# Performance work log

Measured on AMD Instinct MI355X. Metric: run time of the kernel, lower is better.

## Reference

```python
import jax, jax.numpy as jnp
from jax import lax
import numpy as np

QMIN, QMAX = -127.0, 127.0
STRIDE = (1, 1)
PADDING = ((1, 1), (1, 1))
DILATION = (1, 1)
DN = ('NCHW', 'OIHW', 'NCHW')


def _quantize_x(x, scale_x):
    # symmetric static per-tensor int8 quantization
    return jnp.clip(jnp.round(x / scale_x), QMIN, QMAX)


def _quantize_w(w):
    # symmetric dynamic per-output-channel int8 quantization
    scale_w = jnp.max(jnp.abs(w), axis=(1, 2, 3), keepdims=True) / QMAX  # [O,1,1,1]
    q_w = jnp.clip(jnp.round(w / scale_w), QMIN, QMAX)
    return q_w, scale_w


def setup_inputs() -> dict:
    key = jax.random.key(0)
    kx, kw, kb = jax.random.split(key, 3)
    B, C, H, W = 32, 128, 56, 56
    O, kH, kW = 256, 3, 3
    x = jax.random.normal(kx, (B, C, H, W), jnp.float32)
    weight = jax.random.normal(kw, (O, C, kH, kW), jnp.float32) * 0.05
    bias = jax.random.normal(kb, (O,), jnp.float32)
    scale_x = jnp.asarray(0.02, jnp.float32)  # static per-tensor scale buffer
    # exact int8 product lookup table: lut[a+127, b+127] = a*b
    v = np.arange(-127, 128, dtype=np.int32)
    lut = jnp.asarray(v[:, None] * v[None, :])
    return {"x": x, "weight": weight, "bias": bias, "scale_x": scale_x, "lut": lut}


def reference(x, weight, bias, scale_x, lut):
    # lut holds the exact int8 product table, so bgemm_int8(q_x, q_w, lut) is an
    # exact integer GEMM; im2col + bGEMM == conv of quantized tensors.
    q_x = _quantize_x(x, scale_x)            # [B,C,H,W] integer-valued fp32
    q_w, scale_w = _quantize_w(weight)       # [O,C,kH,kW], [O,1,1,1]
    acc = lax.conv_general_dilated(
        q_x, q_w, STRIDE, PADDING, rhs_dilation=DILATION, dimension_numbers=DN
    )                                        # [B,O,OH,OW] integer-valued accumulator
    out = acc * scale_x * scale_w.reshape(1, -1, 1, 1)  # per-channel dequant
    return out + bias.reshape(1, -1, 1, 1)
```

## Files before the change

kernel.cpp:

```cpp
#include <hip/hip_runtime.h>


#define BATCH 32
#define CIN   128
#define HH    56
#define WW    56
#define OCH   256

typedef __attribute__((ext_vector_type(4))) int int4v;
typedef __attribute__((ext_vector_type(2))) long longx2;

#define QX_BYTES (32 * 56 * 56 * 128)
#define QW_BYTES (256 * 1152)
#define WS_NEEDED (QX_BYTES + QW_BYTES + 1024)

__device__ __forceinline__ void gload_lds16(const void* g, void* l) {
  __builtin_amdgcn_global_load_lds(
      (const __attribute__((address_space(1))) unsigned int*)g,
      (__attribute__((address_space(3))) unsigned int*)l, 16, 0, 0);
}

__global__ __launch_bounds__(256) void quant_w_kernel(
    const float* __restrict__ w, const float* __restrict__ sxp,
    char* __restrict__ qwf, float* __restrict__ alpha) {
  __shared__ float wf[1152];
  __shared__ float red[256];
  const int o = blockIdx.x;
  const int tid = threadIdx.x;
  const float* wrow = w + (size_t)o * 1152;
  float m = 0.f;
  for (int i = tid; i < 288; i += 256) {
    const float4 v = ((const float4*)wrow)[i];
    ((float4*)wf)[i] = v;
    m = fmaxf(m, fmaxf(fmaxf(fabsf(v.x), fabsf(v.y)),
                       fmaxf(fabsf(v.z), fabsf(v.w))));
  }
  red[tid] = m;
  __syncthreads();
  for (int s = 128; s > 0; s >>= 1) {
    if (tid < s) red[tid] = fmaxf(red[tid], red[tid + s]);
    __syncthreads();
  }
  const float sc = red[0] / 127.0f;
  if (tid == 0) alpha[o] = sc * sxp[0];
  if (tid < 36) {
    const int r = tid >> 2, c04 = tid & 3;
    const int og = o >> 5, t = (o >> 4) & 1, l16 = o & 15;
    unsigned int* base = (unsigned int*)(qwf + (size_t)og * 36864 +
                                         (size_t)(r * 4 + c04) * 1024);
#pragma unroll
    for (int quad = 0; quad < 4; ++quad) {
#pragma unroll
      for (int half = 0; half < 2; ++half) {
        unsigned int pk = 0;
#pragma unroll
        for (int k = 0; k < 4; ++k) {
          const int c = c04 * 32 + quad * 8 + half * 4 + k;
          const int q =
              (int)fminf(127.f, fmaxf(-127.f, rintf(wf[c * 9 + r] / sc)));
          pk |= ((unsigned int)(q & 255)) << (8 * k);
        }
        base[(l16 * 4 + quad) * 4 + t * 2 + half] = pk;
      }
    }
  }
}

__global__ __launch_bounds__(256) void quant_x_kernel(
    const float* __restrict__ x, const float* __restrict__ sxp,
    unsigned int* __restrict__ qxp) {
  __shared__ char ldsA[128 * 60];
  const int row = blockIdx.x;
  const int b = row / 56, h = row % 56;
  const float sx = sxp[0];
  for (int i = threadIdx.x; i < 1792; i += 256) {
    const int c = i / 14, f = i % 14;
    const float4 v =
        *(const float4*)(x + (((size_t)b * 128 + c) * 56 + h) * 56 + 4 * f);
    unsigned int pk;
    pk  = (unsigned int)((int)fminf(127.f, fmaxf(-127.f, rintf(v.x / sx))) & 255);
    pk |= ((unsigned int)((int)fminf(127.f, fmaxf(-127.f, rintf(v.y / sx))) & 255)) << 8;
    pk |= ((unsigned int)((int)fminf(127.f, fmaxf(-127.f, rintf(v.z / sx))) & 255)) << 16;
    pk |= ((unsigned int)((int)fminf(127.f, fmaxf(-127.f, rintf(v.w / sx))) & 255)) << 24;
    *(unsigned int*)(ldsA + c * 60 + 4 * f) = pk;
  }
  __syncthreads();
  unsigned int* orow = qxp + (size_t)row * 56 * 32;
  for (int i = threadIdx.x; i < 1792; i += 256) {
    const int w = i >> 5, jd = i & 31;
    const int c0 = (jd ^ (((w + 1) & 15) << 1)) << 2;
    unsigned int pk = 0;
#pragma unroll
    for (int k = 0; k < 4; ++k)
      pk |= ((unsigned int)(unsigned char)ldsA[(c0 + k) * 60 + w]) << (8 * k);
    orow[i] = pk;
  }
}

#define XSLAB 8448

__global__ __launch_bounds__(256, 6) void conv_kernel(
    const char* __restrict__ qxp, const char* __restrict__ qwf,
    const float* __restrict__ alpha, const float* __restrict__ bias,
    float* __restrict__ out) {
  __shared__ __attribute__((aligned(16))) char Xs8[3 * XSLAB];

  const int id = blockIdx.x;
  const int xcd = id & 7;
  int kk = id >> 3;
  const int yy = (kk >= 224) ? 1 : 0;
  kk -= yy * 224;
  const int bi = xcd * 224 + kk;
  const int b  = bi / 56;
  const int oh = bi % 56;
  const int o0 = yy * 128;
  const int tid = threadIdx.x;
  const int wave = tid >> 6, lane = tid & 63;
  const int l16 = lane & 15, quad = lane >> 4;

  int m_r[4], n_r[4];
  {
    int4v zz = {0, 0, 0, 0};
    long a1 = 0, b1 = 0, a2 = 0, b2 = 0;
    if (quad == 0) {
      a1 = 1L;
      b1 = (long)(l16 + 1);
      a2 = (long)(l16 + 1);
      b2 = 1L;
    }
    int4v d1 = __builtin_amdgcn_mfma_i32_16x16x32_i8(a1, b1, zz, 0, 0, 0);
    int4v d2 = __builtin_amdgcn_mfma_i32_16x16x32_i8(a2, b2, zz, 0, 0, 0);
#pragma unroll
    for (int r = 0; r < 4; ++r) {
      n_r[r] = (d1[r] - 1) & 15;
      m_r[r] = (d2[r] - 1) & 15;
    }
  }

  const longx2* wb2 = (const longx2*)(qwf + (size_t)(yy * 4 + wave) * 36864) +
                      (l16 * 4 + quad);
  longx2 ap[2][4];
#pragma unroll
  for (int c04 = 0; c04 < 4; ++c04) ap[0][c04] = wb2[(size_t)c04 * 64];

  for (int kh = 0; kh < 3; ++kh) {
    const int ih = oh - 1 + kh;
    char* slab = Xs8 + kh * XSLAB;
    if (ih >= 0 && ih < HH) {
      const char* src = qxp + ((size_t)b * 56 + ih) * 7168;
      for (int i = tid; i < 448; i += 256)
        gload_lds16(src + i * 16, slab + 128 + i * 16);
      for (int i = tid; i < 320; i += 256) {
        const int cg = i >> 5, dw = i & 31;
        const int col = (cg == 0) ? 0 : 56 + cg;
        ((unsigned int*)slab)[col * 32 + dw] = 0u;
      }
    } else {
      for (int i = tid; i < 2112; i += 256) ((unsigned int*)slab)[i] = 0u;
    }
  }

  int4v acc[2][4];
#pragma unroll
  for (int t = 0; t < 2; ++t)
#pragma unroll
    for (int u = 0; u < 4; ++u) acc[t][u] = (int4v){0, 0, 0, 0};

  __syncthreads();

#pragma unroll
  for (int g = 0; g < 9; ++g) {
    const int kh = g / 3, kw = g % 3;
    if (g < 8) {
#pragma unroll
      for (int c04 = 0; c04 < 4; ++c04)
        ap[(g + 1) & 1][c04] = wb2[(size_t)((g + 1) * 4 + c04) * 64];
    }
    const char* Xk = Xs8 + kh * XSLAB;
    const int ph = ((l16 + kw) & 15) << 3;
#pragma unroll
    for (int c04 = 0; c04 < 4; ++c04) {
      const int boff = (c04 * 32 + quad * 8) ^ ph;
      long bop[4];
#pragma unroll
      for (int u = 0; u < 4; ++u)
        bop[u] = *(const long*)(Xk + (u * 16 + l16 + kw) * 128 + boff);
#pragma unroll
      for (int u = 0; u < 4; ++u) {
        acc[0][u] = __builtin_amdgcn_mfma_i32_16x16x32_i8(
            ap[g & 1][c04][0], bop[u], acc[0][u], 0, 0, 0);
        acc[1][u] = __builtin_amdgcn_mfma_i32_16x16x32_i8(
            ap[g & 1][c04][1], bop[u], acc[1][u], 0, 0, 0);
      }
    }
  }

#pragma unroll
  for (int t = 0; t < 2; ++t) {
#pragma unroll
    for (int u = 0; u < 4; ++u) {
#pragma unroll
      for (int r = 0; r < 4; ++r) {
        const int ol = wave * 32 + t * 16 + m_r[r];
        const int ow = u * 16 + n_r[r];
        if (ow < WW) {
          const int oo = o0 + ol;
          out[(((size_t)b * OCH + oo) * HH + oh) * WW + ow] =
              (float)acc[t][u][r] * alpha[oo] + bias[oo];
        }
      }
    }
  }
}

#define FAS_ROW 392
#define FXS_ROW 136
#define FLDS_XS (128 * FAS_ROW)
#define FLDS_SC (FLDS_XS + 66 * FXS_ROW)
#define FLDS_AL (FLDS_SC + 512)
#define FLDS_BI (FLDS_AL + 512)
#define FLDS_RED (FLDS_BI + 512)
#define FLDS_TOT (FLDS_RED + 1024)

__global__ __launch_bounds__(256) void conv_fused_kernel(
    const float* __restrict__ x, const float* __restrict__ w,
    const float* __restrict__ bias, const float* __restrict__ sxp,
    float* __restrict__ out) {
  __shared__ __attribute__((aligned(16))) char lds[FLDS_TOT];
  char* As8 = lds;
  char* Xs8 = lds + FLDS_XS;
  float* scaleS = (float*)(lds + FLDS_SC);
  float* alphaS = (float*)(lds + FLDS_AL);
  float* biasS  = (float*)(lds + FLDS_BI);
  float* red    = (float*)(lds + FLDS_RED);

  const int bi = blockIdx.x;
  const int b  = bi / 56;
  const int oh = bi % 56;
  const int o0 = blockIdx.y * 128;
  const int tid = threadIdx.x;
  const int wave = tid >> 6, lane = tid & 63;
  const int l16 = lane & 15, quad = lane >> 4;
  const float sx = sxp[0];

  int m_r[4], n_r[4];
  {
    int4v zz = {0, 0, 0, 0};
    long a1 = 0, b1 = 0, a2 = 0, b2 = 0;
    if (quad == 0) { a1 = 1L; b1 = (long)(l16 + 1); a2 = (long)(l16 + 1); b2 = 1L; }
    int4v d1 = __builtin_amdgcn_mfma_i32_16x16x32_i8(a1, b1, zz, 0, 0, 0);
    int4v d2 = __builtin_amdgcn_mfma_i32_16x16x32_i8(a2, b2, zz, 0, 0, 0);
#pragma unroll
    for (int r = 0; r < 4; ++r) { n_r[r] = (d1[r] - 1) & 15; m_r[r] = (d2[r] - 1) & 15; }
  }
  {
    const int o = tid >> 1, half = tid & 1;
    const float4* p = (const float4*)(w + (size_t)(o0 + o) * 1152 + half * 576);
    float m = 0.f;
#pragma unroll 4
    for (int i = 0; i < 144; ++i) {
      const float4 v = p[i];
      m = fmaxf(m, fmaxf(fmaxf(fabsf(v.x), fabsf(v.y)), fmaxf(fabsf(v.z), fabsf(v.w))));
    }
    red[tid] = m;
  }
  __syncthreads();
  {
    const int o = tid >> 1;
    if ((tid & 1) == 0) {
      const float sc = fmaxf(red[2 * o], red[2 * o + 1]) / 127.0f;
      scaleS[o] = sc; alphaS[o] = sc * sx; biasS[o] = bias[o0 + o];
    }
  }
  int4v acc[2][4];
#pragma unroll
  for (int t = 0; t < 2; ++t)
#pragma unroll
    for (int u = 0; u < 4; ++u) acc[t][u] = (int4v){0, 0, 0, 0};

  for (int kh = 0; kh < 3; ++kh) {
    const int ih = oh - 1 + kh;
    const bool row_ok = (ih >= 0) && (ih < HH);
    __syncthreads();
    for (int idx = tid; idx < 66 * 128; idx += 256) {
      const int col = idx % 66, c = idx / 66, iw = col - 1;
      int q = 0;
      if (row_ok && iw >= 0 && iw < WW) {
        const float xv = x[(((size_t)b * CIN + c) * HH + ih) * WW + iw];
        q = (int)fminf(127.f, fmaxf(-127.f, rintf(xv / sx)));
      }
      Xs8[col * FXS_ROW + c] = (char)q;
    }
    for (int idx = tid; idx < 16384; idx += 256) {
      const int c = idx & 127, o = idx >> 7;
      const float s = scaleS[o];
      const float* wp = w + (size_t)(o0 + o) * 1152 + c * 9 + kh * 3;
#pragma unroll
      for (int kw = 0; kw < 3; ++kw) {
        const int q = (int)fminf(127.f, fmaxf(-127.f, rintf(wp[kw] / s)));
        As8[o * FAS_ROW + kw * 128 + c] = (char)q;
      }
    }
    __syncthreads();
    const int obase = wave * 32;
#pragma unroll
    for (int kw = 0; kw < 3; ++kw) {
#pragma unroll
      for (int c0 = 0; c0 < 128; c0 += 32) {
        long aop[2], bop[4];
#pragma unroll
        for (int t = 0; t < 2; ++t)
          aop[t] = *(const long*)(As8 + (obase + t * 16 + l16) * FAS_ROW + kw * 128 + c0 + quad * 8);
#pragma unroll
        for (int u = 0; u < 4; ++u)
          bop[u] = *(const long*)(Xs8 + (u * 16 + l16 + kw) * FXS_ROW + c0 + quad * 8);
#pragma unroll
        for (int t = 0; t < 2; ++t)
#pragma unroll
          for (int u = 0; u < 4; ++u)
            acc[t][u] = __builtin_amdgcn_mfma_i32_16x16x32_i8(aop[t], bop[u], acc[t][u], 0, 0, 0);
      }
    }
  }
#pragma unroll
  for (int t = 0; t < 2; ++t) {
#pragma unroll
    for (int u = 0; u < 4; ++u) {
#pragma unroll
      for (int r = 0; r < 4; ++r) {
        const int ol = wave * 32 + t * 16 + m_r[r];
        const int ow = u * 16 + n_r[r];
        if (ow < WW)
          out[(((size_t)b * OCH + o0 + ol) * HH + oh) * WW + ow] =
              (float)acc[t][u][r] * alphaS[ol] + biasS[ol];
      }
    }
  }
}

extern "C" void kernel_launch(void* const* d_in, const int* in_sizes, int n_in,
                              void* d_out, int out_size, void* d_ws, size_t ws_size,
                              hipStream_t stream) {
  const float *x = nullptr, *w = nullptr, *bias = nullptr, *sx = nullptr;
  for (int i = 0; i < n_in; ++i) {
    const int s = in_sizes[i];
    if (s == BATCH * CIN * HH * WW) x = (const float*)d_in[i];
    else if (s == OCH * CIN * 9)    w = (const float*)d_in[i];
    else if (s == OCH)              bias = (const float*)d_in[i];
    else if (s == 1)                sx = (const float*)d_in[i];
  }
  if (!x || !w || !bias || !sx) {
    x = (const float*)d_in[0]; w = (const float*)d_in[1];
    bias = (const float*)d_in[2]; sx = (const float*)d_in[3];
  }
  float* out = (float*)d_out;

  if (ws_size >= (size_t)WS_NEEDED) {
    unsigned int* qxp = (unsigned int*)d_ws;
    char* qwf = (char*)d_ws + QX_BYTES;
    float* alpha = (float*)((char*)d_ws + QX_BYTES + QW_BYTES);
    quant_w_kernel<<<OCH, 256, 0, stream>>>(w, sx, qwf, alpha);
    quant_x_kernel<<<BATCH * HH, 256, 0, stream>>>(x, sx, qxp);
    conv_kernel<<<BATCH * HH * 2, 256, 0, stream>>>(
        (const char*)qxp, qwf, alpha, bias, out);
  } else {
    conv_fused_kernel<<<dim3(BATCH * HH, 2), 256, 0, stream>>>(x, w, bias, sx, out);
  }
}
```

Measured before the change: 196.9 us.

## Switch conv to 32x32x32 int8 MFMA with full-channel blocks and new weight layout

Replaces the 16x16x32 int8 MFMA tiles with 32x32x32 int8 MFMA. Each block now computes all 256 output channels for one output row, so the grid is halved and each input slab is loaded into LDS once instead of twice. The packed weight layout in quant_w_kernel changes to match the new A-operand fragment, and launch bounds drop to 3 blocks per CU. Each wave now holds 64 channels and 64 accumulator registers, which raises register pressure and reduces the number of resident blocks.

```diff
diff --git a/kernel.cpp b/kernel.cpp
--- a/kernel.cpp
+++ b/kernel.cpp
@@ -8,6 +8,7 @@
 #define OCH   256
 
 typedef __attribute__((ext_vector_type(4))) int int4v;
+typedef __attribute__((ext_vector_type(16))) int int16v;
 typedef __attribute__((ext_vector_type(2))) long longx2;
 
 #define QX_BYTES (32 * 56 * 56 * 128)
@@ -43,26 +44,24 @@
   }
   const float sc = red[0] / 127.0f;
   if (tid == 0) alpha[o] = sc * sxp[0];
-  if (tid < 36) {
-    const int r = tid >> 2, c04 = tid & 3;
-    const int og = o >> 5, t = (o >> 4) & 1, l16 = o & 15;
-    unsigned int* base = (unsigned int*)(qwf + (size_t)og * 36864 +
-                                         (size_t)(r * 4 + c04) * 1024);
-#pragma unroll
-    for (int quad = 0; quad < 4; ++quad) {
-#pragma unroll
-      for (int half = 0; half < 2; ++half) {
-        unsigned int pk = 0;
-#pragma unroll
-        for (int k = 0; k < 4; ++k) {
-          const int c = c04 * 32 + quad * 8 + half * 4 + k;
-          const int q =
-              (int)fminf(127.f, fmaxf(-127.f, rintf(wf[c * 9 + r] / sc)));
-          pk |= ((unsigned int)(q & 255)) << (8 * k);
-        }
-        base[(l16 * 4 + quad) * 4 + t * 2 + half] = pk;
-      }
-    }
+  if (tid < 72) {
+    const int r = tid >> 3, cs = (tid >> 1) & 3, hi = tid & 1;
+    const int ot = o >> 5, ml = o & 31;
+    int4v pk;
+#pragma unroll
+    for (int d = 0; d < 4; ++d) {
+      unsigned int p = 0;
+#pragma unroll
+      for (int k = 0; k < 4; ++k) {
+        const int c = cs * 32 + hi * 16 + d * 4 + k;
+        const int q =
+            (int)fminf(127.f, fmaxf(-127.f, rintf(wf[c * 9 + r] / sc)));
+        p |= ((unsigned int)(q & 255)) << (8 * k);
+      }
+      pk[d] = (int)p;
+    }
+    *(int4v*)(qwf +
+              ((((size_t)ot * 9 + r) * 4 + cs) * 64 + ml + 32 * hi) * 16) = pk;
   }
 }
 
@@ -99,7 +98,7 @@
 
 #define XSLAB 8448
 
-__global__ __launch_bounds__(256, 6) void conv_kernel(
+__global__ __launch_bounds__(256, 3) void conv_kernel(
     const char* __restrict__ qxp, const char* __restrict__ qwf,
     const float* __restrict__ alpha, const float* __restrict__ bias,
     float* __restrict__ out) {
@@ -107,41 +106,12 @@
 
   const int id = blockIdx.x;
   const int xcd = id & 7;
-  int kk = id >> 3;
-  const int yy = (kk >= 224) ? 1 : 0;
-  kk -= yy * 224;
-  const int bi = xcd * 224 + kk;
+  const int bi = xcd * 224 + (id >> 3);
   const int b  = bi / 56;
   const int oh = bi % 56;
-  const int o0 = yy * 128;
   const int tid = threadIdx.x;
   const int wave = tid >> 6, lane = tid & 63;
-  const int l16 = lane & 15, quad = lane >> 4;
-
-  int m_r[4], n_r[4];
-  {
-    int4v zz = {0, 0, 0, 0};
-    long a1 = 0, b1 = 0, a2 = 0, b2 = 0;
-    if (quad == 0) {
-      a1 = 1L;
-      b1 = (long)(l16 + 1);
-      a2 = (long)(l16 + 1);
-      b2 = 1L;
-    }
-    int4v d1 = __builtin_amdgcn_mfma_i32_16x16x32_i8(a1, b1, zz, 0, 0, 0);
-    int4v d2 = __builtin_amdgcn_mfma_i32_16x16x32_i8(a2, b2, zz, 0, 0, 0);
-#pragma unroll
-    for (int r = 0; r < 4; ++r) {
-      n_r[r] = (d1[r] - 1) & 15;
-      m_r[r] = (d2[r] - 1) & 15;
-    }
-  }
-
-  const longx2* wb2 = (const longx2*)(qwf + (size_t)(yy * 4 + wave) * 36864) +
-                      (l16 * 4 + quad);
-  longx2 ap[2][4];
-#pragma unroll
-  for (int c04 = 0; c04 < 4; ++c04) ap[0][c04] = wb2[(size_t)c04 * 64];
+  const int l31 = lane & 31, hi = lane >> 5;
 
   for (int kh = 0; kh < 3; ++kh) {
     const int ih = oh - 1 + kh;
@@ -160,11 +130,22 @@
     }
   }
 
-  int4v acc[2][4];
-#pragma unroll
-  for (int t = 0; t < 2; ++t)
-#pragma unroll
-    for (int u = 0; u < 4; ++u) acc[t][u] = (int4v){0, 0, 0, 0};
+  const int4v* wb = (const int4v*)qwf;
+  const int ot0 = wave * 2;
+  int4v ap[2][2][4];
+#pragma unroll
+  for (int ot = 0; ot < 2; ++ot)
+#pragma unroll
+    for (int cs = 0; cs < 4; ++cs)
+      ap[0][ot][cs] = wb[(((size_t)(ot0 + ot) * 9 + 0) * 4 + cs) * 64 + lane];
+
+  int16v acc[2][2];
+#pragma unroll
+  for (int ot = 0; ot < 2; ++ot)
+#pragma unroll
+    for (int u = 0; u < 2; ++u)
+#pragma unroll
+      for (int r = 0; r < 16; ++r) acc[ot][u][r] = 0;
 
   __syncthreads();
 
@@ -173,41 +154,48 @@
     const int kh = g / 3, kw = g % 3;
     if (g < 8) {
 #pragma unroll
-      for (int c04 = 0; c04 < 4; ++c04)
-        ap[(g + 1) & 1][c04] = wb2[(size_t)((g + 1) * 4 + c04) * 64];
+      for (int ot = 0; ot < 2; ++ot)
+#pragma unroll
+        for (int cs = 0; cs < 4; ++cs)
+          ap[(g + 1) & 1][ot][cs] =
+              wb[(((size_t)(ot0 + ot) * 9 + (g + 1)) * 4 + cs) * 64 + lane];
     }
     const char* Xk = Xs8 + kh * XSLAB;
-    const int ph = ((l16 + kw) & 15) << 3;
-#pragma unroll
-    for (int c04 = 0; c04 < 4; ++c04) {
-      const int boff = (c04 * 32 + quad * 8) ^ ph;
-      long bop[4];
-#pragma unroll
-      for (int u = 0; u < 4; ++u)
-        bop[u] = *(const long*)(Xk + (u * 16 + l16 + kw) * 128 + boff);
-#pragma unroll
-      for (int u = 0; u < 4; ++u) {
-        acc[0][u] = __builtin_amdgcn_mfma_i32_16x16x32_i8(
-            ap[g & 1][c04][0], bop[u], acc[0][u], 0, 0, 0);
-        acc[1][u] = __builtin_amdgcn_mfma_i32_16x16x32_i8(
-            ap[g & 1][c04][1], bop[u], acc[1][u], 0, 0, 0);
-      }
-    }
-  }
-
-#pragma unroll
-  for (int t = 0; t < 2; ++t) {
-#pragma unroll
-    for (int u = 0; u < 4; ++u) {
-#pragma unroll
-      for (int r = 0; r < 4; ++r) {
-        const int ol = wave * 32 + t * 16 + m_r[r];
-        const int ow = u * 16 + n_r[r];
-        if (ow < WW) {
-          const int oo = o0 + ol;
-          out[(((size_t)b * OCH + oo) * HH + oh) * WW + ow] =
-              (float)acc[t][u][r] * alpha[oo] + bias[oo];
-        }
+    const int ph = ((l31 + kw) & 15) << 3;
+#pragma unroll
+    for (int cs = 0; cs < 4; ++cs) {
+      int4v bop[2];
+#pragma unroll
+      for (int u = 0; u < 2; ++u) {
+        const int col = u * 32 + l31 + kw;
+        const int base = (cs * 32 + hi * 16) ^ ph;
+        longx2 q;
+        q[0] = *(const long*)(Xk + col * 128 + base);
+        q[1] = *(const long*)(Xk + col * 128 + (base ^ 8));
+        bop[u] = __builtin_bit_cast(int4v, q);
+      }
+#pragma unroll
+      for (int ot = 0; ot < 2; ++ot)
+#pragma unroll
+        for (int u = 0; u < 2; ++u)
+          acc[ot][u] = __builtin_amdgcn_mfma_i32_32x32x32_i8(
+              ap[g & 1][ot][cs], bop[u], acc[ot][u], 0, 0, 0);
+    }
+  }
+
+#pragma unroll
+  for (int ot = 0; ot < 2; ++ot) {
+    const int obase = wave * 64 + ot * 32;
+#pragma unroll
+    for (int r = 0; r < 16; ++r) {
+      const int o = obase + (r & 3) + 8 * (r >> 2) + 4 * hi;
+      const float al = alpha[o], bz = bias[o];
+#pragma unroll
+      for (int u = 0; u < 2; ++u) {
+        const int ow = u * 32 + l31;
+        if (ow < WW)
+          out[(((size_t)b * OCH + o) * HH + oh) * WW + ow] =
+              (float)acc[ot][u][r] * al + bz;
       }
     }
   }
@@ -361,7 +349,7 @@
     float* alpha = (float*)((char*)d_ws + QX_BYTES + QW_BYTES);
     quant_w_kernel<<<OCH, 256, 0, stream>>>(w, sx, qwf, alpha);
     quant_x_kernel<<<BATCH * HH, 256, 0, stream>>>(x, sx, qxp);
-    conv_kernel<<<BATCH * HH * 2, 256, 0, stream>>>(
+    conv_kernel<<<BATCH * HH, 256, 0, stream>>>(
         (const char*)qxp, qwf, alpha, bias, out);
   } else {
     conv_fused_kernel<<<dim3(BATCH * HH, 2), 256, 0, stream>>>(x, w, bias, sx, out);
```

After: 204.2 us. 1.04x slower.
